# Kernel tuning notes

Measured on AMD Instinct MI355X. Metric: run time of the kernel, lower is better.

Reference implementation:

```python
import jax, jax.numpy as jnp
import numpy as np

N_NODES = 20000
N_EDGES = 640000
D_IN = 128
D_OUT = 128


def setup_inputs() -> dict:
    key = jax.random.key(0)
    k1, k2, k3, k4 = jax.random.split(key, 4)
    x = jax.random.normal(k1, (N_NODES, D_IN), dtype=jnp.float32)
    edge_index = jax.random.randint(k2, (2, N_EDGES), 0, N_NODES, dtype=jnp.int64)
    edge_weight = jnp.ones((N_EDGES,), dtype=jnp.float32)
    # Linear(in_feats, out_feats) params (PyTorch convention: W [out, in])
    bound = 1.0 / np.sqrt(D_IN)
    W = jax.random.uniform(k3, (D_OUT, D_IN), minval=-bound, maxval=bound, dtype=jnp.float32)
    b = jax.random.uniform(k4, (D_OUT,), minval=-bound, maxval=bound, dtype=jnp.float32)
    return {"x": x, "edge_index": edge_index, "edge_weight": edge_weight, "W": W, "b": b}


def reference(x, edge_index, edge_weight, W, b):
    # MeanAggregator: h = Linear(x); out = row-normalized spmm(adj, h)
    h = x @ W.T + b  # [N, D_OUT]
    row, col = edge_index[0], edge_index[1]
    # message = w_ij * h[j], scattered into row i  (spmm with COO adjacency)
    msg = h[col] * edge_weight[:, None]  # [E, D_OUT]
    agg = jax.ops.segment_sum(msg, row, num_segments=N_NODES)  # [N, D_OUT]
    deg = jax.ops.segment_sum(edge_weight, row, num_segments=N_NODES)  # [N]
    deg_inv = jnp.where(deg > 0, 1.0 / deg, 0.0)
    out = agg * deg_inv[:, None]
    # normalize=True -> F.normalize(out, p=2, dim=-1)
    norm = jnp.linalg.norm(out, axis=-1, keepdims=True)
    out = out / jnp.maximum(norm, 1e-12)
    return out
```

## Files before the change

### kernel.cpp

```cpp
#include <hip/hip_runtime.h>
#include <hip/hip_bf16.h>
#include <math.h>

#define N_NODES 20000
#define N_EDGES 640000
#define D 128

#define BSHIFT 5
#define BNODES 32
#define NBUCK 625
#define CAP 1536
#define HNOD 16
#define HCAP 768
#define AGG_T 512
#define SRPT 3
#define NBLK1 320
#define CHUNK 2000
#define GPAD 16
#define CASTBLK 2500

#define GROWS 16

typedef __attribute__((ext_vector_type(8))) short bf16x8;
typedef __attribute__((ext_vector_type(4))) float f32x4;

static __device__ __forceinline__ unsigned short f2bf(float f) {
  unsigned u = __float_as_uint(f);
  return (unsigned short)((u + 0x7fffu + ((u >> 16) & 1u)) >> 16);
}
static __device__ __forceinline__ float bflo(unsigned v) {
  return __uint_as_float(v << 16);
}
static __device__ __forceinline__ float bfhi(unsigned v) {
  return __uint_as_float(v & 0xffff0000u);
}

__global__ __launch_bounds__(256) void zero_kernel(int* __restrict__ p, int n) {
  const int i = blockIdx.x * 256 + threadIdx.x;
  if (i < n) p[i] = 0;
}

__global__ __launch_bounds__(256) void castbin_kernel(
    const float* __restrict__ x, const float* __restrict__ W,
    const int* __restrict__ rows, const int* __restrict__ cols,
    const float* __restrict__ ew,
    unsigned* __restrict__ xb, unsigned* __restrict__ Wb,
    int* __restrict__ gcur, uint2* __restrict__ bins) {
  __shared__ int cnt[NBUCK];
  __shared__ int basep[NBUCK];
  const int tid = threadIdx.x;
  if (blockIdx.x < NBLK1) {
    const int e0 = blockIdx.x * CHUNK;
    for (int i = tid; i < NBUCK; i += 256) cnt[i] = 0;
    __syncthreads();
    const int4* r4 = reinterpret_cast<const int4*>(rows + e0);
    for (int t = tid; t < CHUNK / 4; t += 256) {
      const int4 rv = r4[t];
      atomicAdd(&cnt[rv.x >> BSHIFT], 1);
      atomicAdd(&cnt[rv.y >> BSHIFT], 1);
      atomicAdd(&cnt[rv.z >> BSHIFT], 1);
      atomicAdd(&cnt[rv.w >> BSHIFT], 1);
    }
    __syncthreads();
    for (int i = tid; i < NBUCK; i += 256) {
      const int c = cnt[i];
      basep[i] = c ? atomicAdd(&gcur[i * GPAD], c) : 0;
    }
    __syncthreads();
    for (int i = tid; i < NBUCK; i += 256) cnt[i] = 0;
    __syncthreads();
    for (int t = tid; t < CHUNK / 4; t += 256) {
      const int4 rv = r4[t];
      const int4 cv = reinterpret_cast<const int4*>(cols + e0)[t];
      const float4 wv = reinterpret_cast<const float4*>(ew + e0)[t];
      const int rr[4] = {rv.x, rv.y, rv.z, rv.w};
      const int cc[4] = {cv.x, cv.y, cv.z, cv.w};
      const float ww[4] = {wv.x, wv.y, wv.z, wv.w};
#pragma unroll
      for (int u = 0; u < 4; ++u) {
        const int b = rr[u] >> BSHIFT;
        const int p = basep[b] + atomicAdd(&cnt[b], 1);
        if (p < CAP)
          bins[(size_t)b * CAP + p] =
              make_uint2(((unsigned)(rr[u] & (BNODES - 1)) << 16) | (unsigned)cc[u],
                         __float_as_uint(ww[u]));
      }
    }
  } else {
    const int i = (blockIdx.x - NBLK1) * 256 + tid;
    if (i < N_NODES * D / 4) {
      const float4 v = *reinterpret_cast<const float4*>(&x[(size_t)i * 4]);
      uint2 o;
      o.x = (unsigned)f2bf(v.x) | ((unsigned)f2bf(v.y) << 16);
      o.y = (unsigned)f2bf(v.z) | ((unsigned)f2bf(v.w) << 16);
      *reinterpret_cast<uint2*>(&xb[(size_t)i * 2]) = o;
    }
    if (i < D * D / 4) {
      const float4 v = *reinterpret_cast<const float4*>(&W[(size_t)i * 4]);
      uint2 o;
      o.x = (unsigned)f2bf(v.x) | ((unsigned)f2bf(v.y) << 16);
      o.y = (unsigned)f2bf(v.z) | ((unsigned)f2bf(v.w) << 16);
      *reinterpret_cast<uint2*>(&Wb[(size_t)i * 2]) = o;
    }
  }
}

__global__ __launch_bounds__(AGG_T) void agg_gemm_kernel(
    const unsigned* __restrict__ xb, const int* __restrict__ gcur,
    const uint2* __restrict__ bins, const unsigned* __restrict__ Wb,
    const float* __restrict__ bias, float* __restrict__ out) {
  __shared__ uint2 list[HCAP];
  __shared__ unsigned aggls[HNOD * 64];
  __shared__ int cnt[HNOD];
  __shared__ int base[HNOD];
  __shared__ float degls[HNOD];
  const int b = blockIdx.x >> 1;
  const int half = blockIdx.x & 1;
  const int tid = threadIdx.x;
  const int n = min(gcur[b * GPAD], CAP);
  if (tid < HNOD) cnt[tid] = 0;
  __syncthreads();

  uint2 ebuf[SRPT];
  int rkbuf[SRPT], rlbuf[SRPT];
#pragma unroll
  for (int j = 0; j < SRPT; ++j) {
    const int i = tid + j * AGG_T;
    rlbuf[j] = -1;
    if (i < n) {
      const uint2 e = bins[(size_t)b * CAP + i];
      const int rl = (int)(e.x >> 16);
      if ((rl >> 4) == half) {
        ebuf[j] = e;
        rlbuf[j] = rl & 15;
        rkbuf[j] = atomicAdd(&cnt[rl & 15], 1);
      }
    }
  }
  __syncthreads();
  if (tid < 64) {
    const int c = (tid < HNOD) ? cnt[tid] : 0;
    int s = c;
#pragma unroll
    for (int off = 1; off < HNOD; off <<= 1) {
      const int t = __shfl_up(s, off);
      if (tid >= off) s += t;
    }
    if (tid < HNOD) base[tid] = s - c;
  }
  __syncthreads();
#pragma unroll
  for (int j = 0; j < SRPT; ++j)
    if (rlbuf[j] >= 0) {
      const int p = base[rlbuf[j]] + rkbuf[j];
      if (p < HCAP) list[p] = ebuf[j];
    }
  __syncthreads();

  const int wv = tid >> 6, lane = tid & 63;
  const int q4 = lane >> 4, fidx = lane & 15;
  for (int q = 0; q < 2; ++q) {
    const int rl = wv * 2 + q;
    const int s = base[rl];
    const int ke = min(s + cnt[rl], HCAP);
    float a[8] = {0.f, 0.f, 0.f, 0.f, 0.f, 0.f, 0.f, 0.f};
    float dw = 0.f;
    for (int k = s; k < ke; k += 32) {
      uint4 v[8];
      float w[8];
#pragma unroll
      for (int u = 0; u < 8; ++u) {
        int idx = k + u * 4 + q4;
        const bool ok = idx < ke;
        if (!ok) idx = ke - 1;
        const uint2 e = list[idx];
        w[u] = ok ? __uint_as_float(e.y) : 0.f;
        v[u] = *reinterpret_cast<const uint4*>(
            &xb[(size_t)(e.x & 0xffffu) * (D / 2) + fidx * 4]);
      }
#pragma unroll
      for (int u = 0; u < 8; ++u) {
        a[0] += bflo(v[u].x) * w[u]; a[1] += bfhi(v[u].x) * w[u];
        a[2] += bflo(v[u].y) * w[u]; a[3] += bfhi(v[u].y) * w[u];
        a[4] += bflo(v[u].z) * w[u]; a[5] += bfhi(v[u].z) * w[u];
        a[6] += bflo(v[u].w) * w[u]; a[7] += bfhi(v[u].w) * w[u];
        dw += w[u];
      }
    }
#pragma unroll
    for (int j = 0; j < 8; ++j) {
      a[j] += __shfl_xor(a[j], 16);
      a[j] += __shfl_xor(a[j], 32);
    }
    dw += __shfl_xor(dw, 16);
    dw += __shfl_xor(dw, 32);
    const float dinv = dw > 0.f ? 1.f / dw : 0.f;
    if (lane == 0) degls[rl] = dw;
    if (q4 == 0) {
      uint4 o;
      o.x = (unsigned)f2bf(a[0] * dinv) | ((unsigned)f2bf(a[1] * dinv) << 16);
      o.y = (unsigned)f2bf(a[2] * dinv) | ((unsigned)f2bf(a[3] * dinv) << 16);
      o.z = (unsigned)f2bf(a[4] * dinv) | ((unsigned)f2bf(a[5] * dinv) << 16);
      o.w = (unsigned)f2bf(a[6] * dinv) | ((unsigned)f2bf(a[7] * dinv) << 16);
      *reinterpret_cast<uint4*>(
          &aggls[rl * 64 + ((fidx * 4) ^ ((rl & 7) << 2))]) = o;
    }
  }
  __syncthreads();

  if (wv != 0) return;
  const int arow = lane & 15;
  const int koff = (lane >> 4) * 4;

  bf16x8 afr[4];
#pragma unroll
  for (int kk = 0; kk < 4; ++kk) {
    const int wbase = (kk * 16 + koff) ^ ((arow & 7) << 2);
    union { uint4 u; bf16x8 v; } cv;
    cv.u = *reinterpret_cast<const uint4*>(&aggls[arow * 64 + wbase]);
    afr[kk] = cv.v;
  }

  f32x4 acc[8];
#pragma unroll
  for (int t = 0; t < 8; ++t) {
    const int o = t * 16 + (lane & 15);
    f32x4 c = {0.f, 0.f, 0.f, 0.f};
#pragma unroll
    for (int kk = 0; kk < 4; ++kk) {
      union { uint4 u; bf16x8 v; } cv;
      cv.u = *reinterpret_cast<const uint4*>(
          &Wb[(size_t)o * (D / 2) + kk * 16 + koff]);
      c = __builtin_amdgcn_mfma_f32_16x16x32_bf16(afr[kk], cv.v, c, 0, 0, 0);
    }
    acc[t] = c;
  }

  float ss[4] = {0.f, 0.f, 0.f, 0.f};
#pragma unroll
  for (int t = 0; t < 8; ++t) {
    const float bc = bias[t * 16 + (lane & 15)];
#pragma unroll
    for (int r = 0; r < 4; ++r) {
      const float y = acc[t][r] + bc;
      acc[t][r] = y;
      ss[r] += y * y;
    }
  }
#pragma unroll
  for (int r = 0; r < 4; ++r) {
#pragma unroll
    for (int off = 1; off < 16; off <<= 1)
      ss[r] += __shfl_xor(ss[r], off);
  }
  const int row0 = b * BNODES + half * HNOD;
  float scale[4];
#pragma unroll
  for (int r = 0; r < 4; ++r) {
    const int lrow = (lane >> 4) * 4 + r;
    const float dw = degls[lrow];
    scale[r] = (dw > 0.f) ? 1.f / fmaxf(sqrtf(ss[r]), 1e-12f) : 0.f;
  }
#pragma unroll
  for (int t = 0; t < 8; ++t) {
#pragma unroll
    for (int r = 0; r < 4; ++r) {
      const int lrow = (lane >> 4) * 4 + r;
      out[(size_t)(row0 + lrow) * D + t * 16 + (lane & 15)] =
          acc[t][r] * scale[r];
    }
  }
}

__global__ __launch_bounds__(256) void scatter_kernel(
    const float* __restrict__ x, const int* __restrict__ rows,
    const int* __restrict__ cols, const float* __restrict__ ew,
    float* __restrict__ out, float* __restrict__ degw) {
  const int e = blockIdx.x * 4 + (threadIdx.x >> 6);
  const int lane = threadIdx.x & 63;
  if (e >= N_EDGES) return;
  const int r = rows[e];
  const int c = cols[e];
  const float w = ew[e];
  const float2 v = *reinterpret_cast<const float2*>(&x[(size_t)c * D + lane * 2]);
  atomicAdd(&out[(size_t)r * D + lane * 2], v.x * w);
  atomicAdd(&out[(size_t)r * D + lane * 2 + 1], v.y * w);
  if (lane == 0) atomicAdd(&degw[r], w);
}

__global__ __launch_bounds__(256) void linear_norm_kernel(
    const float* __restrict__ W, const float* __restrict__ b,
    const float* __restrict__ degw, float* __restrict__ out) {
  __shared__ float Ws[D][D + 1];
  __shared__ float xs[GROWS][D];
  __shared__ float dws[GROWS];
  const int tid = threadIdx.x;
  const int row0 = blockIdx.x * GROWS;
  for (int idx = tid; idx < D * D; idx += 256)
    Ws[idx >> 7][idx & 127] = W[idx];
  if (tid < GROWS) dws[tid] = degw[row0 + tid];
  __syncthreads();
  for (int idx = tid; idx < GROWS * D; idx += 256) {
    const int r = idx >> 7;
    const float dw = dws[r];
    const float dinv = dw > 0.f ? 1.f / dw : 0.f;
    xs[r][idx & 127] = out[(size_t)(row0 + r) * D + (idx & 127)] * dinv;
  }
  __syncthreads();
  const int o = tid & 127;
  const int rh = tid >> 7;
  float acc[GROWS / 2];
#pragma unroll
  for (int j = 0; j < GROWS / 2; ++j) acc[j] = 0.f;
  for (int k = 0; k < D; ++k) {
    const float wv = Ws[o][k];
#pragma unroll
    for (int j = 0; j < GROWS / 2; ++j)
      acc[j] += xs[rh + 2 * j][k] * wv;
  }
  const float bias = b[o];
  __syncthreads();
#pragma unroll
  for (int j = 0; j < GROWS / 2; ++j)
    xs[rh + 2 * j][o] = acc[j] + bias;
  __syncthreads();
  const int w = tid >> 6, lane = tid & 63;
#pragma unroll
  for (int q = 0; q < 4; ++q) {
    const int r = w * 4 + q;
    const float2 v = *reinterpret_cast<const float2*>(&xs[r][lane * 2]);
    float ss = v.x * v.x + v.y * v.y;
#pragma unroll
    for (int off = 1; off < 64; off <<= 1) ss += __shfl_xor(ss, off);
    const float dw = dws[r];
    const float scale = (dw > 0.f) ? 1.f / fmaxf(sqrtf(ss), 1e-12f) : 0.f;
    *reinterpret_cast<float2*>(&out[(size_t)(row0 + r) * D + lane * 2]) =
        make_float2(v.x * scale, v.y * scale);
  }
}

extern "C" void kernel_launch(void* const* d_in, const int* in_sizes, int n_in,
                              void* d_out, int out_size, void* d_ws, size_t ws_size,
                              hipStream_t stream) {
  const float* x  = (const float*)d_in[0];
  const int*   ei = (const int*)d_in[1];
  const float* ew = (const float*)d_in[2];
  const float* W  = (const float*)d_in[3];
  const float* b  = (const float*)d_in[4];
  float* out = (float*)d_out;
  char* ws = (char*)d_ws;

  const int* rows = ei;
  const int* cols = ei + N_EDGES;

  size_t off = 0;
  int* gcur = (int*)(ws + off);        off += (size_t)NBUCK * GPAD * 4;
  float* degw = (float*)(ws + off);    off += (size_t)N_NODES * 4;
  unsigned* xb = (unsigned*)(ws + off);  off += (size_t)N_NODES * (D / 2) * 4;
  unsigned* Wb = (unsigned*)(ws + off);  off += (size_t)D * (D / 2) * 4;
  uint2* bins = (uint2*)(ws + off);    off += (size_t)NBUCK * CAP * 8;
  const size_t main_bytes = off;
  const size_t fallback_bytes = (size_t)NBUCK * GPAD * 4 + (size_t)N_NODES * 4;

  if (ws_size >= main_bytes) {
    zero_kernel<<<(NBUCK * GPAD + 255) / 256, 256, 0, stream>>>(gcur, NBUCK * GPAD);
    castbin_kernel<<<NBLK1 + CASTBLK, 256, 0, stream>>>(x, W, rows, cols, ew,
                                                        xb, Wb, gcur, bins);
    agg_gemm_kernel<<<NBUCK * 2, AGG_T, 0, stream>>>(xb, gcur, bins, Wb, b, out);
  } else if (ws_size >= fallback_bytes) {
    hipMemsetAsync(out, 0, (size_t)N_NODES * D * 4, stream);
    hipMemsetAsync(degw, 0, (size_t)N_NODES * 4, stream);
    scatter_kernel<<<(N_EDGES + 3) / 4, 256, 0, stream>>>(x, rows, cols, ew, out, degw);
    linear_norm_kernel<<<N_NODES / GROWS, 256, 0, stream>>>(W, b, degw, out);
  }
}
```

Baseline: 63.30 us.

## Bin edges into 16-node buckets and keep edge chunk in registers

Halves the bucket width so each aggregation block owns exactly one 16-node bucket. Blocks no longer both read a 32-node bucket and discard the half that is not theirs, so bins are read once with vectorized uint4 loads. The binning pass now keeps the rows, cols and weights it loads in registers between the counting and scattering passes, instead of reloading them from global memory. The trade-offs are twice as many global bucket counters and atomics, larger shared histograms per binning block, and a lower per-bucket capacity (768) that risks overflow. Removing the HCAP clamp on the list end also assumes no bucket overflows.

```diff
diff --git a/kernel.cpp b/kernel.cpp
--- a/kernel.cpp
+++ b/kernel.cpp
@@ -6,14 +6,11 @@
 #define N_EDGES 640000
 #define D 128
 
-#define BSHIFT 5
-#define BNODES 32
-#define NBUCK 625
-#define CAP 1536
-#define HNOD 16
-#define HCAP 768
+#define BSHIFT 4
+#define BNODES 16
+#define NB2 1250
+#define CAP2 768
 #define AGG_T 512
-#define SRPT 3
 #define NBLK1 320
 #define CHUNK 2000
 #define GPAD 16
@@ -46,42 +43,45 @@
     const float* __restrict__ ew,
     unsigned* __restrict__ xb, unsigned* __restrict__ Wb,
     int* __restrict__ gcur, uint2* __restrict__ bins) {
-  __shared__ int cnt[NBUCK];
-  __shared__ int basep[NBUCK];
+  __shared__ int cnt[NB2];
+  __shared__ int basep[NB2];
   const int tid = threadIdx.x;
   if (blockIdx.x < NBLK1) {
     const int e0 = blockIdx.x * CHUNK;
-    for (int i = tid; i < NBUCK; i += 256) cnt[i] = 0;
+    for (int i = tid; i < NB2; i += 256) cnt[i] = 0;
     __syncthreads();
+    int4 rv[2], cv[2];
+    float4 wv[2];
+    int nslot = 0;
     const int4* r4 = reinterpret_cast<const int4*>(rows + e0);
     for (int t = tid; t < CHUNK / 4; t += 256) {
-      const int4 rv = r4[t];
-      atomicAdd(&cnt[rv.x >> BSHIFT], 1);
-      atomicAdd(&cnt[rv.y >> BSHIFT], 1);
-      atomicAdd(&cnt[rv.z >> BSHIFT], 1);
-      atomicAdd(&cnt[rv.w >> BSHIFT], 1);
+      rv[nslot] = r4[t];
+      cv[nslot] = reinterpret_cast<const int4*>(cols + e0)[t];
+      wv[nslot] = reinterpret_cast<const float4*>(ew + e0)[t];
+      atomicAdd(&cnt[rv[nslot].x >> BSHIFT], 1);
+      atomicAdd(&cnt[rv[nslot].y >> BSHIFT], 1);
+      atomicAdd(&cnt[rv[nslot].z >> BSHIFT], 1);
+      atomicAdd(&cnt[rv[nslot].w >> BSHIFT], 1);
+      ++nslot;
     }
     __syncthreads();
-    for (int i = tid; i < NBUCK; i += 256) {
+    for (int i = tid; i < NB2; i += 256) {
       const int c = cnt[i];
       basep[i] = c ? atomicAdd(&gcur[i * GPAD], c) : 0;
     }
     __syncthreads();
-    for (int i = tid; i < NBUCK; i += 256) cnt[i] = 0;
+    for (int i = tid; i < NB2; i += 256) cnt[i] = 0;
     __syncthreads();
-    for (int t = tid; t < CHUNK / 4; t += 256) {
-      const int4 rv = r4[t];
-      const int4 cv = reinterpret_cast<const int4*>(cols + e0)[t];
-      const float4 wv = reinterpret_cast<const float4*>(ew + e0)[t];
-      const int rr[4] = {rv.x, rv.y, rv.z, rv.w};
-      const int cc[4] = {cv.x, cv.y, cv.z, cv.w};
-      const float ww[4] = {wv.x, wv.y, wv.z, wv.w};
+    for (int sl = 0; sl < nslot; ++sl) {
+      const int rr[4] = {rv[sl].x, rv[sl].y, rv[sl].z, rv[sl].w};
+      const int cc[4] = {cv[sl].x, cv[sl].y, cv[sl].z, cv[sl].w};
+      const float ww[4] = {wv[sl].x, wv[sl].y, wv[sl].z, wv[sl].w};
 #pragma unroll
       for (int u = 0; u < 4; ++u) {
         const int b = rr[u] >> BSHIFT;
         const int p = basep[b] + atomicAdd(&cnt[b], 1);
-        if (p < CAP)
-          bins[(size_t)b * CAP + p] =
+        if (p < CAP2)
+          bins[(size_t)b * CAP2 + p] =
               make_uint2(((unsigned)(rr[u] & (BNODES - 1)) << 16) | (unsigned)cc[u],
                          __float_as_uint(ww[u]));
       }
@@ -109,52 +109,47 @@
     const unsigned* __restrict__ xb, const int* __restrict__ gcur,
     const uint2* __restrict__ bins, const unsigned* __restrict__ Wb,
     const float* __restrict__ bias, float* __restrict__ out) {
-  __shared__ uint2 list[HCAP];
-  __shared__ unsigned aggls[HNOD * 64];
-  __shared__ int cnt[HNOD];
-  __shared__ int base[HNOD];
-  __shared__ float degls[HNOD];
-  const int b = blockIdx.x >> 1;
-  const int half = blockIdx.x & 1;
+  __shared__ uint2 list[CAP2];
+  __shared__ unsigned aggls[BNODES * 64];
+  __shared__ int cnt[BNODES];
+  __shared__ int base[BNODES];
+  __shared__ float degls[BNODES];
+  const int b = blockIdx.x;
   const int tid = threadIdx.x;
-  const int n = min(gcur[b * GPAD], CAP);
-  if (tid < HNOD) cnt[tid] = 0;
-  __syncthreads();
-
-  uint2 ebuf[SRPT];
-  int rkbuf[SRPT], rlbuf[SRPT];
-#pragma unroll
-  for (int j = 0; j < SRPT; ++j) {
-    const int i = tid + j * AGG_T;
-    rlbuf[j] = -1;
-    if (i < n) {
-      const uint2 e = bins[(size_t)b * CAP + i];
-      const int rl = (int)(e.x >> 16);
-      if ((rl >> 4) == half) {
-        ebuf[j] = e;
-        rlbuf[j] = rl & 15;
-        rkbuf[j] = atomicAdd(&cnt[rl & 15], 1);
+  const int n = min(gcur[b * GPAD], CAP2);
+  if (tid < BNODES) cnt[tid] = 0;
+  __syncthreads();
+
+  uint2 e0v, e1v;
+  int rk0 = -1, rk1 = -1, rl0 = 0, rl1 = 0;
+  {
+    const int i0 = tid * 2;
+    if (i0 < n) {
+      const uint4 p = *reinterpret_cast<const uint4*>(&bins[(size_t)b * CAP2 + i0]);
+      e0v = make_uint2(p.x, p.y);
+      rl0 = (int)(p.x >> 16);
+      rk0 = atomicAdd(&cnt[rl0], 1);
+      if (i0 + 1 < n) {
+        e1v = make_uint2(p.z, p.w);
+        rl1 = (int)(p.z >> 16);
+        rk1 = atomicAdd(&cnt[rl1], 1);
       }
     }
   }
   __syncthreads();
   if (tid < 64) {
-    const int c = (tid < HNOD) ? cnt[tid] : 0;
+    const int c = (tid < BNODES) ? cnt[tid] : 0;
     int s = c;
 #pragma unroll
-    for (int off = 1; off < HNOD; off <<= 1) {
+    for (int off = 1; off < BNODES; off <<= 1) {
       const int t = __shfl_up(s, off);
       if (tid >= off) s += t;
     }
-    if (tid < HNOD) base[tid] = s - c;
-  }
-  __syncthreads();
-#pragma unroll
-  for (int j = 0; j < SRPT; ++j)
-    if (rlbuf[j] >= 0) {
-      const int p = base[rlbuf[j]] + rkbuf[j];
-      if (p < HCAP) list[p] = ebuf[j];
-    }
+    if (tid < BNODES) base[tid] = s - c;
+  }
+  __syncthreads();
+  if (rk0 >= 0) list[base[rl0] + rk0] = e0v;
+  if (rk1 >= 0) list[base[rl1] + rk1] = e1v;
   __syncthreads();
 
   const int wv = tid >> 6, lane = tid & 63;
@@ -162,7 +157,7 @@
   for (int q = 0; q < 2; ++q) {
     const int rl = wv * 2 + q;
     const int s = base[rl];
-    const int ke = min(s + cnt[rl], HCAP);
+    const int ke = s + cnt[rl];
     float a[8] = {0.f, 0.f, 0.f, 0.f, 0.f, 0.f, 0.f, 0.f};
     float dw = 0.f;
     for (int k = s; k < ke; k += 32) {
@@ -253,7 +248,7 @@
     for (int off = 1; off < 16; off <<= 1)
       ss[r] += __shfl_xor(ss[r], off);
   }
-  const int row0 = b * BNODES + half * HNOD;
+  const int row0 = b * BNODES;
   float scale[4];
 #pragma unroll
   for (int r = 0; r < 4; ++r) {
@@ -354,19 +349,19 @@
   const int* cols = ei + N_EDGES;
 
   size_t off = 0;
-  int* gcur = (int*)(ws + off);        off += (size_t)NBUCK * GPAD * 4;
+  int* gcur = (int*)(ws + off);        off += (size_t)NB2 * GPAD * 4;
   float* degw = (float*)(ws + off);    off += (size_t)N_NODES * 4;
   unsigned* xb = (unsigned*)(ws + off);  off += (size_t)N_NODES * (D / 2) * 4;
   unsigned* Wb = (unsigned*)(ws + off);  off += (size_t)D * (D / 2) * 4;
-  uint2* bins = (uint2*)(ws + off);    off += (size_t)NBUCK * CAP * 8;
+  uint2* bins = (uint2*)(ws + off);    off += (size_t)NB2 * CAP2 * 8;
   const size_t main_bytes = off;
-  const size_t fallback_bytes = (size_t)NBUCK * GPAD * 4 + (size_t)N_NODES * 4;
+  const size_t fallback_bytes = (size_t)NB2 * GPAD * 4 + (size_t)N_NODES * 4;
 
   if (ws_size >= main_bytes) {
-    zero_kernel<<<(NBUCK * GPAD + 255) / 256, 256, 0, stream>>>(gcur, NBUCK * GPAD);
+    zero_kernel<<<(NB2 * GPAD + 255) / 256, 256, 0, stream>>>(gcur, NB2 * GPAD);
     castbin_kernel<<<NBLK1 + CASTBLK, 256, 0, stream>>>(x, W, rows, cols, ew,
                                                         xb, Wb, gcur, bins);
-    agg_gemm_kernel<<<NBUCK * 2, AGG_T, 0, stream>>>(xb, gcur, bins, Wb, b, out);
+    agg_gemm_kernel<<<NB2, AGG_T, 0, stream>>>(xb, gcur, bins, Wb, b, out);
   } else if (ws_size >= fallback_bytes) {
     hipMemsetAsync(out, 0, (size_t)N_NODES * D * 4, stream);
     hipMemsetAsync(degw, 0, (size_t)N_NODES * 4, stream);
```

Measured after the change: 75.50 us. 19.3% more time.

## Stage binned edges in LDS and write buckets contiguously to global

Applied to the files above, without the earlier changes.

The binning pass now does a local prefix scan of per-bucket counts and sorts each block's edges into a shared-memory staging buffer. It then writes them out in bucket order, so global stores to the bins array are contiguous runs instead of scattered 8-byte writes. The chunk size per block doubles and the block count halves, which lowers the number of global atomics on bucket cursors but also halves parallelism and adds 32KB of LDS per block. The full row index is now packed into the edge word, and the consumer masks it back to the local 5-bit index.

```diff
diff --git a/kernel.cpp b/kernel.cpp
--- a/kernel.cpp
+++ b/kernel.cpp
@@ -14,8 +14,8 @@
 #define HCAP 768
 #define AGG_T 512
 #define SRPT 3
-#define NBLK1 320
-#define CHUNK 2000
+#define NBLK1 160
+#define CHUNK 4000
 #define GPAD 16
 #define CASTBLK 2500
 
@@ -46,8 +46,10 @@
     const float* __restrict__ ew,
     unsigned* __restrict__ xb, unsigned* __restrict__ Wb,
     int* __restrict__ gcur, uint2* __restrict__ bins) {
+  __shared__ uint2 stage[CHUNK];
   __shared__ int cnt[NBUCK];
-  __shared__ int basep[NBUCK];
+  __shared__ int lbase[NBUCK];
+  __shared__ int gbase[NBUCK];
   const int tid = threadIdx.x;
   if (blockIdx.x < NBLK1) {
     const int e0 = blockIdx.x * CHUNK;
@@ -62,9 +64,24 @@
       atomicAdd(&cnt[rv.w >> BSHIFT], 1);
     }
     __syncthreads();
+    if (tid < 64) {
+      int carry = 0;
+      for (int c0 = 0; c0 < NBUCK; c0 += 64) {
+        const int idx = c0 + tid;
+        const int v = (idx < NBUCK) ? cnt[idx] : 0;
+        int s = v;
+#pragma unroll
+        for (int off = 1; off < 64; off <<= 1) {
+          const int t = __shfl_up(s, off);
+          if (tid >= off) s += t;
+        }
+        if (idx < NBUCK) lbase[idx] = carry + s - v;
+        carry += __shfl(s, 63);
+      }
+    }
     for (int i = tid; i < NBUCK; i += 256) {
       const int c = cnt[i];
-      basep[i] = c ? atomicAdd(&gcur[i * GPAD], c) : 0;
+      gbase[i] = c ? atomicAdd(&gcur[i * GPAD], c) : 0;
     }
     __syncthreads();
     for (int i = tid; i < NBUCK; i += 256) cnt[i] = 0;
@@ -79,12 +96,18 @@
 #pragma unroll
       for (int u = 0; u < 4; ++u) {
         const int b = rr[u] >> BSHIFT;
-        const int p = basep[b] + atomicAdd(&cnt[b], 1);
-        if (p < CAP)
-          bins[(size_t)b * CAP + p] =
-              make_uint2(((unsigned)(rr[u] & (BNODES - 1)) << 16) | (unsigned)cc[u],
-                         __float_as_uint(ww[u]));
-      }
+        const int r = atomicAdd(&cnt[b], 1);
+        stage[lbase[b] + r] =
+            make_uint2(((unsigned)rr[u] << 16) | (unsigned)cc[u],
+                       __float_as_uint(ww[u]));
+      }
+    }
+    __syncthreads();
+    for (int i = tid; i < CHUNK; i += 256) {
+      const uint2 e = stage[i];
+      const int b = (int)(e.x >> 21);
+      const int p = gbase[b] + (i - lbase[b]);
+      if (p < CAP) bins[(size_t)b * CAP + p] = e;
     }
   } else {
     const int i = (blockIdx.x - NBLK1) * 256 + tid;
@@ -129,11 +152,11 @@
     rlbuf[j] = -1;
     if (i < n) {
       const uint2 e = bins[(size_t)b * CAP + i];
-      const int rl = (int)(e.x >> 16);
-      if ((rl >> 4) == half) {
+      const int rl32 = (int)(e.x >> 16) & 31;
+      if ((rl32 >> 4) == half) {
         ebuf[j] = e;
-        rlbuf[j] = rl & 15;
-        rkbuf[j] = atomicAdd(&cnt[rl & 15], 1);
+        rlbuf[j] = rl32 & 15;
+        rkbuf[j] = atomicAdd(&cnt[rl32 & 15], 1);
       }
     }
   }
```

Result: faster. 59.31 us (-6.3%).
